# Performance work log

Hardware: AMD Instinct MI355X
Metric: run time of the kernel (lower is better)

## Reference

```python
import jax, jax.numpy as jnp
import numpy as np

H, HEADS, LAYERS = 512, 4, 3
HD = H // HEADS
FFN = 4 * H
B, S = 4, 2048
EPS = 1e-5
SCALE_BASE = 512.0
GAMMAS = (1.0 - np.exp(np.linspace(np.log(1.0 / 32.0), np.log(1.0 / 512.0), HEADS))).astype(np.float32)


def _xpos(x, downscale):
    # x: [B, heads, L, d]; standard XPOS rotary with per-dim decay scale
    L, d = x.shape[-2], x.shape[-1]
    half = d // 2
    s = (jnp.arange(half, dtype=jnp.float32) + 0.4 * d) / (1.4 * d)          # [half]
    pos = jnp.arange(L, dtype=jnp.float32)
    scale = s[None, :] ** (pos[:, None] / SCALE_BASE)                         # [L, half]
    inv_freq = 1.0 / (10000.0 ** (jnp.arange(half, dtype=jnp.float32) / half))
    ang = pos[:, None] * inv_freq[None, :]                                    # [L, half]
    if downscale:
        scale = 1.0 / scale
    sin_s = jnp.repeat(jnp.sin(ang) * scale, 2, axis=-1)                      # [L, d]
    cos_s = jnp.repeat(jnp.cos(ang) * scale, 2, axis=-1)
    x1, x2 = x[..., 0::2], x[..., 1::2]
    rot = jnp.stack([-x2, x1], axis=-1).reshape(x.shape)                      # rotate_every_two
    return x * cos_s + rot * sin_s


def _layernorm(x, w, b):
    m = x.mean(-1, keepdims=True)
    v = ((x - m) ** 2).mean(-1, keepdims=True)
    return (x - m) / jnp.sqrt(v + EPS) * w + b


def _decay_mask(L):
    n = jnp.arange(L)
    nm = n[:, None] - n[None, :]
    g = jnp.asarray(GAMMAS)                                                   # [heads]
    # D[h,n,m] = gamma_h^(n-m) for n>=m else 0
    return jnp.where((nm >= 0)[None], g[:, None, None] ** jnp.maximum(nm, 0)[None], 0.0)


def _msr(X, WQ, WK, WV, WG, WO, gnw, gnb, D):
    # X: [B,S,H]; WQ/WK/WV: [heads,H,HD]; D: [heads,S,S]
    Q = _xpos(jnp.einsum('bsh,nhd->bnsd', X, WQ), False)
    K = _xpos(jnp.einsum('bsh,nhd->bnsd', X, WK), True)
    V = jnp.einsum('bsh,nhd->bnsd', X, WV)
    A = jnp.einsum('bnsd,bntd->bnst', Q, K) * D[None]                          # decay-weighted retention
    Y = jnp.einsum('bnst,bntd->bnsd', A, V)                                    # [B,heads,S,HD]
    Y = jnp.transpose(Y, (0, 2, 1, 3))                                         # [B,S,heads,HD] (head-major concat)
    m = Y.mean(-1, keepdims=True)
    v = ((Y - m) ** 2).mean(-1, keepdims=True)
    Yn = ((Y - m) / jnp.sqrt(v + EPS)).reshape(X.shape[0], X.shape[1], H) * gnw + gnb  # GroupNorm(heads, H)
    G = X @ WG
    return (G * jax.nn.sigmoid(G) * Yn) @ WO                                   # swish gate + out proj


def setup_inputs() -> dict:
    key = jax.random.key(0)
    ks = jax.random.split(key, 10)
    rn = lambda k, shape, sc: jax.random.normal(k, shape, jnp.float32) * sc
    return {
        'X': rn(ks[0], (B, S, H), 1.0),
        'WQ': rn(ks[1], (LAYERS, HEADS, H, HD), 1.0 / H),
        'WK': rn(ks[2], (LAYERS, HEADS, H, HD), 1.0 / H),
        'WV': rn(ks[3], (LAYERS, HEADS, H, HD), 1.0 / H),
        'WG': rn(ks[4], (LAYERS, H, H), 1.0 / H),
        'WO': rn(ks[5], (LAYERS, H, H), 1.0 / H),
        'gn_w': jnp.ones((LAYERS, H), jnp.float32),
        'gn_b': jnp.zeros((LAYERS, H), jnp.float32),
        'ln1_w': jnp.ones((LAYERS, H), jnp.float32),
        'ln1_b': jnp.zeros((LAYERS, H), jnp.float32),
        'ln2_w': jnp.ones((LAYERS, H), jnp.float32),
        'ln2_b': jnp.zeros((LAYERS, H), jnp.float32),
        'ffn_w1': rn(ks[6], (LAYERS, H, FFN), (2.0 / (H + FFN)) ** 0.5),
        'ffn_b1': jnp.zeros((LAYERS, FFN), jnp.float32),
        'ffn_w2': rn(ks[7], (LAYERS, FFN, H), (2.0 / (H + FFN)) ** 0.5),
        'ffn_b2': jnp.zeros((LAYERS, H), jnp.float32),
    }


def reference(X, WQ, WK, WV, WG, WO, gn_w, gn_b, ln1_w, ln1_b, ln2_w, ln2_b, ffn_w1, ffn_b1, ffn_w2, ffn_b2):
    D = _decay_mask(X.shape[1])
    for l in range(LAYERS):
        Y = _msr(_layernorm(X, ln1_w[l], ln1_b[l]), WQ[l], WK[l], WV[l], WG[l], WO[l], gn_w[l], gn_b[l], D) + X
        Hn = _layernorm(Y, ln2_w[l], ln2_b[l])
        X = jax.nn.gelu(Hn @ ffn_w1[l] + ffn_b1[l], approximate=False) @ ffn_w2[l] + ffn_b2[l] + Y
    return X, jnp.einsum('bsh,bth->bst', X, X)
```

## Files before the change

### kernel.cpp

```cpp
#include <hip/hip_runtime.h>
#include <math.h>

#define HH 512
#define NHEADS 4
#define HD 128
#define HALF 64
#define FFND 2048
#define BB 4
#define SS 2048
#define NLAYERS 3
#define ROWS (BB*SS)
#define EPSF 1e-5f

typedef float f32x4 __attribute__((ext_vector_type(4)));
typedef __bf16 bf16x8 __attribute__((ext_vector_type(8)));

__device__ __forceinline__ unsigned short f2bf(float f) {
    union { float f; unsigned u; } v; v.f = f;
    unsigned r = (v.u + 0x7FFFu + ((v.u >> 16) & 1u)) >> 16;
    return (unsigned short)r;
}
__device__ __forceinline__ float bf2f(unsigned short h) {
    union { unsigned u; float f; } v; v.u = ((unsigned)h) << 16;
    return v.f;
}
__device__ __forceinline__ void gl16(const void* g, void* l) {
    __builtin_amdgcn_global_load_lds((const __attribute__((address_space(1))) void*)g,
                                     (__attribute__((address_space(3))) void*)l, 16, 0, 0);
}
__device__ __forceinline__ bf16x8 ld8(const void* p) { return *(const bf16x8*)p; }

__global__ void k_tables(float* __restrict__ cq, float* __restrict__ sq,
                         float* __restrict__ ck, float* __restrict__ sk) {
    int i = threadIdx.x;
    int s = blockIdx.x;
    float si   = ((float)i + 0.4f * (float)HD) / (1.4f * (float)HD);
    float scale = powf(si, (float)s / 512.0f);
    float invf = powf(10000.0f, -((float)i) / (float)HALF);
    float ang  = (float)s * invf;
    float c = cosf(ang), sn = sinf(ang);
    int idx = s * HALF + i;
    cq[idx] = c * scale;   sq[idx] = sn * scale;
    float is = 1.0f / scale;
    ck[idx] = c * is;      sk[idx] = sn * is;
}

__global__ __launch_bounds__(256) void k_wt(const float* __restrict__ src, unsigned short* __restrict__ dst,
                                            int K, int N) {
    __shared__ float T[32][33];
    int n0 = blockIdx.x * 32, k0 = blockIdx.y * 32;
    size_t mb = (size_t)blockIdx.z * (size_t)K * N;
    src += mb; dst += mb;
    int tx = threadIdx.x & 31, ty = threadIdx.x >> 5;
    #pragma unroll
    for (int i = 0; i < 4; ++i) {
        int r = ty + i * 8;
        T[r][tx] = src[(size_t)(k0 + r) * N + n0 + tx];
    }
    __syncthreads();
    #pragma unroll
    for (int i = 0; i < 4; ++i) {
        int r = ty + i * 8;
        dst[(size_t)(n0 + r) * K + k0 + tx] = f2bf(T[tx][r]);
    }
}

__global__ __launch_bounds__(256) void k_ln(const float* __restrict__ x, const float* __restrict__ w,
                                            const float* __restrict__ b, unsigned short* __restrict__ y) {
    int lane = threadIdx.x & 63;
    size_t row = (size_t)blockIdx.x * 4 + (threadIdx.x >> 6);
    const float4* xr = (const float4*)(x + row * HH);
    float4 v0 = xr[lane * 2];
    float4 v1 = xr[lane * 2 + 1];
    float s  = v0.x + v0.y + v0.z + v0.w + v1.x + v1.y + v1.z + v1.w;
    float ss = v0.x*v0.x + v0.y*v0.y + v0.z*v0.z + v0.w*v0.w
             + v1.x*v1.x + v1.y*v1.y + v1.z*v1.z + v1.w*v1.w;
    for (int off = 32; off > 0; off >>= 1) {
        s  += __shfl_xor(s, off);
        ss += __shfl_xor(ss, off);
    }
    float m   = s * (1.0f / HH);
    float var = ss * (1.0f / HH) - m * m;
    float inv = rsqrtf(var + EPSF);
    int h0 = lane * 8;
    float4 wa = *(const float4*)(w + h0);
    float4 wb = *(const float4*)(w + h0 + 4);
    float4 ba = *(const float4*)(b + h0);
    float4 bb2 = *(const float4*)(b + h0 + 4);
    unsigned short o0 = f2bf((v0.x - m) * inv * wa.x + ba.x);
    unsigned short o1 = f2bf((v0.y - m) * inv * wa.y + ba.y);
    unsigned short o2 = f2bf((v0.z - m) * inv * wa.z + ba.z);
    unsigned short o3 = f2bf((v0.w - m) * inv * wa.w + ba.w);
    unsigned short o4 = f2bf((v1.x - m) * inv * wb.x + bb2.x);
    unsigned short o5 = f2bf((v1.y - m) * inv * wb.y + bb2.y);
    unsigned short o6 = f2bf((v1.z - m) * inv * wb.z + bb2.z);
    unsigned short o7 = f2bf((v1.w - m) * inv * wb.w + bb2.w);
    uint4 pk;
    pk.x = o0 | ((unsigned)o1 << 16);
    pk.y = o2 | ((unsigned)o3 << 16);
    pk.z = o4 | ((unsigned)o5 << 16);
    pk.w = o6 | ((unsigned)o7 << 16);
    *(uint4*)(y + row * HH + h0) = pk;
}

__global__ __launch_bounds__(256) void k_xpos(unsigned short* __restrict__ Q, unsigned short* __restrict__ Kp,
    const float* __restrict__ cq, const float* __restrict__ sq,
    const float* __restrict__ ck, const float* __restrict__ sk) {
    int row = blockIdx.x, p = threadIdx.x;
    int s = row & (SS - 1), i = p & (HALF - 1);
    int ti = s * HALF + i;
    size_t off = (size_t)row * HH + p * 2;
    unsigned qv = *(unsigned*)(Q + off);
    float x1 = bf2f(qv & 0xffff), x2 = bf2f(qv >> 16);
    float c = cq[ti], sn = sq[ti];
    unsigned short e = f2bf(x1 * c - x2 * sn), o = f2bf(x2 * c + x1 * sn);
    *(unsigned*)(Q + off) = (unsigned)e | ((unsigned)o << 16);
    unsigned kv = *(unsigned*)(Kp + off);
    x1 = bf2f(kv & 0xffff); x2 = bf2f(kv >> 16);
    c = ck[ti]; sn = sk[ti];
    e = f2bf(x1 * c - x2 * sn); o = f2bf(x2 * c + x1 * sn);
    *(unsigned*)(Kp + off) = (unsigned)e | ((unsigned)o << 16);
}

__global__ __launch_bounds__(256) void k_ret(
    const unsigned short* __restrict__ Q, const unsigned short* __restrict__ K,
    const unsigned short* __restrict__ V, float* __restrict__ Y) {
    __shared__ __align__(16) char sm[57344];
    const int tid = threadIdx.x;
    const int lane = tid & 63, wid = tid >> 6;
    const int lcol = lane & 15, lrow = lane >> 4;
    const int xs = blockIdx.x, hn = blockIdx.y, b = blockIdx.z;
    const int s0 = xs * 64;
    const double la = -3.4657359027997265, lb = -6.238324625039508;
    const float gamma = (float)(1.0 - exp(la + (lb - la) * ((double)hn / 3.0)));
    const float l2g = log2f(gamma);
    const size_t rowbase = (size_t)b * SS;
    const size_t colbase = (size_t)hn * HD;
    #pragma unroll
    for (int c = 0; c < 4; ++c) {
        int chunk = wid * 4 + c;
        int r = chunk * 4 + lrow;
        int w = ((lane & 15) * 16) ^ ((r & 7) << 4);
        gl16((const char*)Q + ((rowbase + s0 + r) * HH + colbase) * 2 + w, sm + chunk * 1024);
    }
    float gr[4], gni[4];
    #pragma unroll
    for (int j = 0; j < 4; ++j) { gr[j] = exp2f(l2g * (float)j); gni[j] = exp2f(-l2g * (16.0f * j)); }
    f32x4 accy[8];
    #pragma unroll
    for (int i = 0; i < 8; ++i) accy[i] = f32x4{0.f, 0.f, 0.f, 0.f};
    const int nt = xs + 1;
    for (int t = 0; t < nt; ++t) {
        const int t0 = t * 64;
        __syncthreads();
        #pragma unroll
        for (int c = 0; c < 4; ++c) {
            int chunk = wid * 4 + c;
            int r = chunk * 4 + lrow;
            int w = ((lane & 15) * 16) ^ ((r & 7) << 4);
            gl16((const char*)K + ((rowbase + t0 + r) * HH + colbase) * 2 + w, sm + 16384 + chunk * 1024);
        }
        {
            const int tt = tid & 63, q4 = tid >> 6;
            #pragma unroll
            for (int j = 0; j < 4; ++j) {
                const int d0 = q4 * 32 + j * 8;
                uint4 vv = *(const uint4*)((const char*)V + ((rowbase + t0 + tt) * HH + colbase + d0) * 2);
                const unsigned short* vs = (const unsigned short*)&vv;
                #pragma unroll
                for (int e = 0; e < 8; ++e) {
                    int d = d0 + e;
                    *(unsigned short*)(sm + 32768 + d * 128 + ((tt * 2) ^ ((d & 7) << 4))) = vs[e];
                }
            }
        }
        __syncthreads();
        f32x4 pacc[4];
        #pragma unroll
        for (int i = 0; i < 4; ++i) pacc[i] = f32x4{0.f, 0.f, 0.f, 0.f};
        #pragma unroll
        for (int kk = 0; kk < 4; ++kk) {
            int ar = wid * 16 + lcol;
            bf16x8 af = ld8(sm + ar * 256 + ((kk * 64 + lrow * 16) ^ ((ar & 7) << 4)));
            #pragma unroll
            for (int nn = 0; nn < 4; ++nn) {
                int br = nn * 16 + lcol;
                bf16x8 bf = ld8(sm + 16384 + br * 256 + ((kk * 64 + lrow * 16) ^ ((br & 7) << 4)));
                pacc[nn] = __builtin_amdgcn_mfma_f32_16x16x32_bf16(af, bf, pacc[nn], 0, 0, 0);
            }
        }
        const int e0 = (s0 - t0) + wid * 16 + lrow * 4 - lcol;
        const float G0 = exp2f(l2g * (float)e0);
        #pragma unroll
        for (int nn = 0; nn < 4; ++nn) {
            #pragma unroll
            for (int j = 0; j < 4; ++j) {
                const int delta = e0 + j - nn * 16;
                const float dd = (delta >= 0) ? (G0 * gr[j] * gni[nn]) : 0.0f;
                const float pv = pacc[nn][j] * dd;
                const int pr = wid * 16 + lrow * 4 + j;
                const int pc = nn * 16 + lcol;
                *(unsigned short*)(sm + 49152 + pr * 128 + ((pc * 2) ^ ((pr & 7) << 4))) = f2bf(pv);
            }
        }
        #pragma unroll
        for (int ks = 0; ks < 2; ++ks) {
            int ar = wid * 16 + lcol;
            bf16x8 pf = ld8(sm + 49152 + ar * 128 + ((ks * 64 + lrow * 16) ^ ((ar & 7) << 4)));
            #pragma unroll
            for (int nn = 0; nn < 8; ++nn) {
                int dr = nn * 16 + lcol;
                bf16x8 vf = ld8(sm + 32768 + dr * 128 + ((ks * 64 + lrow * 16) ^ ((dr & 7) << 4)));
                accy[nn] = __builtin_amdgcn_mfma_f32_16x16x32_bf16(pf, vf, accy[nn], 0, 0, 0);
            }
        }
    }
    #pragma unroll
    for (int nn = 0; nn < 8; ++nn)
        #pragma unroll
        for (int j = 0; j < 4; ++j) {
            size_t row = rowbase + s0 + wid * 16 + lrow * 4 + j;
            Y[row * HH + colbase + nn * 16 + lcol] = accy[nn][j];
        }
}

__global__ __launch_bounds__(256) void k_gate(
    const float* __restrict__ Yr, const unsigned short* __restrict__ G,
    const float* __restrict__ gw, const float* __restrict__ gb,
    unsigned short* __restrict__ E) {
    int lane = threadIdx.x & 63;
    int grp  = blockIdx.x * 4 + (threadIdx.x >> 6);
    int row = grp >> 2, nh = grp & 3;
    size_t off = (size_t)row * HH + nh * HD + lane * 2;
    float2 v = *(const float2*)(Yr + off);
    float s = v.x + v.y, ss = v.x * v.x + v.y * v.y;
    for (int o = 32; o > 0; o >>= 1) {
        s  += __shfl_xor(s, o);
        ss += __shfl_xor(ss, o);
    }
    float m   = s * (1.0f / HD);
    float var = ss * (1.0f / HD) - m * m;
    float inv = rsqrtf(var + EPSF);
    int h = nh * HD + lane * 2;
    unsigned gv = *(const unsigned*)(G + off);
    float g0 = bf2f(gv & 0xffff), g1 = bf2f(gv >> 16);
    float2 w2 = *(const float2*)(gw + h), b2 = *(const float2*)(gb + h);
    float yn0 = (v.x - m) * inv * w2.x + b2.x;
    float yn1 = (v.y - m) * inv * w2.y + b2.y;
    float e0v = g0 / (1.0f + expf(-g0)) * yn0;
    float e1v = g1 / (1.0f + expf(-g1)) * yn1;
    *(unsigned*)(E + off) = (unsigned)f2bf(e0v) | ((unsigned)f2bf(e1v) << 16);
}

__global__ __launch_bounds__(256) void k_cast(const float* __restrict__ x, unsigned short* __restrict__ y) {
    size_t i = ((size_t)blockIdx.x * 256 + threadIdx.x) * 8;
    float4 a = *(const float4*)(x + i), c = *(const float4*)(x + i + 4);
    uint4 pk;
    pk.x = f2bf(a.x) | ((unsigned)f2bf(a.y) << 16);
    pk.y = f2bf(a.z) | ((unsigned)f2bf(a.w) << 16);
    pk.z = f2bf(c.x) | ((unsigned)f2bf(c.y) << 16);
    pk.w = f2bf(c.z) | ((unsigned)f2bf(c.w) << 16);
    *(uint4*)(y + i) = pk;
}

template<int EPI, int OUTBF>
__global__ __launch_bounds__(256) void k_mm(
    const unsigned short* __restrict__ A, const unsigned short* __restrict__ Bt,
    void* __restrict__ Cv, const float* __restrict__ bias, const float* __restrict__ Rs,
    int M, int N, int K, size_t aB, size_t bB, size_t cB) {
    __shared__ __align__(16) char sm[16384];
    const int tid = threadIdx.x;
    const int lane = tid & 63, wid = tid >> 6;
    const int wr = wid >> 1, wc = wid & 1;
    const int lcol = lane & 15, lrow = lane >> 4;
    const size_t m0 = (size_t)blockIdx.x * 128, n0 = (size_t)blockIdx.y * 128;
    const char* Ab = (const char*)(A + (size_t)blockIdx.z * aB);
    const char* Bb = (const char*)(Bt + (size_t)blockIdx.z * bB);
    f32x4 acc[4][4];
    #pragma unroll
    for (int i = 0; i < 4; ++i)
        #pragma unroll
        for (int j = 0; j < 4; ++j) acc[i][j] = f32x4{0.f, 0.f, 0.f, 0.f};
    for (int k0 = 0; k0 < K; k0 += 32) {
        __syncthreads();
        #pragma unroll
        for (int c = 0; c < 2; ++c) {
            int chunk = wid * 2 + c;
            int r = chunk * 16 + (lane >> 2);
            int w = ((lane & 3) ^ (r & 3)) << 4;
            gl16(Ab + ((size_t)(m0 + r) * K + k0) * 2 + w, sm + chunk * 1024);
            gl16(Bb + ((size_t)(n0 + r) * K + k0) * 2 + w, sm + 8192 + chunk * 1024);
        }
        __syncthreads();
        bf16x8 af[4], bfr[4];
        #pragma unroll
        for (int m = 0; m < 4; ++m) {
            int r = wr * 64 + m * 16 + lcol;
            af[m] = ld8(sm + r * 64 + ((lrow * 16) ^ ((r & 3) << 4)));
        }
        #pragma unroll
        for (int n2 = 0; n2 < 4; ++n2) {
            int r = wc * 64 + n2 * 16 + lcol;
            bfr[n2] = ld8(sm + 8192 + r * 64 + ((lrow * 16) ^ ((r & 3) << 4)));
        }
        #pragma unroll
        for (int m = 0; m < 4; ++m)
            #pragma unroll
            for (int n2 = 0; n2 < 4; ++n2)
                acc[m][n2] = __builtin_amdgcn_mfma_f32_16x16x32_bf16(af[m], bfr[n2], acc[m][n2], 0, 0, 0);
    }
    float* Cf = (float*)Cv + (size_t)blockIdx.z * cB;
    unsigned short* Cb = (unsigned short*)Cv + (size_t)blockIdx.z * cB;
    const float* Rb = (EPI >= 2) ? (Rs + (size_t)blockIdx.z * cB) : nullptr;
    #pragma unroll
    for (int m = 0; m < 4; ++m) {
        #pragma unroll
        for (int n2 = 0; n2 < 4; ++n2) {
            size_t col = n0 + wc * 64 + n2 * 16 + lcol;
            float bc = (EPI == 1 || EPI == 2) ? bias[col] : 0.0f;
            #pragma unroll
            for (int j = 0; j < 4; ++j) {
                size_t row = m0 + wr * 64 + m * 16 + lrow * 4 + j;
                float v = acc[m][n2][j];
                if (EPI == 1) { v += bc; v = 0.5f * v * (1.0f + erff(v * 0.70710678118654752f)); }
                else if (EPI == 2) v += bc + Rb[row * N + col];
                else if (EPI == 3) v += Rb[row * N + col];
                if (OUTBF) Cb[row * N + col] = f2bf(v);
                else       Cf[row * N + col] = v;
            }
        }
    }
}

extern "C" void kernel_launch(void* const* d_in, const int* in_sizes, int n_in,
                              void* d_out, int out_size, void* d_ws, size_t ws_size,
                              hipStream_t stream) {
    const float* X0  = (const float*)d_in[0];
    const float* WQ  = (const float*)d_in[1];
    const float* WK  = (const float*)d_in[2];
    const float* WV  = (const float*)d_in[3];
    const float* WG  = (const float*)d_in[4];
    const float* WO  = (const float*)d_in[5];
    const float* gnw = (const float*)d_in[6];
    const float* gnb = (const float*)d_in[7];
    const float* l1w = (const float*)d_in[8];
    const float* l1b = (const float*)d_in[9];
    const float* l2w = (const float*)d_in[10];
    const float* l2b = (const float*)d_in[11];
    const float* fw1 = (const float*)d_in[12];
    const float* fb1 = (const float*)d_in[13];
    const float* fw2 = (const float*)d_in[14];
    const float* fb2 = (const float*)d_in[15];
    float* outX = (float*)d_out;
    float* outG = outX + (size_t)ROWS * HH;

    char* wp = (char*)d_ws;
    auto take = [&](size_t bytes) { char* p = wp; wp += (bytes + 255) & ~(size_t)255; return p; };
    float* cq = (float*)take((size_t)SS * HALF * 4);
    float* sq = (float*)take((size_t)SS * HALF * 4);
    float* ck = (float*)take((size_t)SS * HALF * 4);
    float* sk = (float*)take((size_t)SS * HALF * 4);
    unsigned short* WQt = (unsigned short*)take((size_t)NLAYERS * HH * HH * 2);
    unsigned short* WKt = (unsigned short*)take((size_t)NLAYERS * HH * HH * 2);
    unsigned short* WVt = (unsigned short*)take((size_t)NLAYERS * HH * HH * 2);
    unsigned short* WGt = (unsigned short*)take((size_t)NLAYERS * HH * HH * 2);
    unsigned short* WOt = (unsigned short*)take((size_t)NLAYERS * HH * HH * 2);
    unsigned short* F1t = (unsigned short*)take((size_t)NLAYERS * HH * FFND * 2);
    unsigned short* F2t = (unsigned short*)take((size_t)NLAYERS * HH * FFND * 2);
    unsigned short* Xn  = (unsigned short*)take((size_t)ROWS * HH * 2);
    unsigned short* Qb  = (unsigned short*)take((size_t)ROWS * HH * 2);
    unsigned short* Kb  = (unsigned short*)take((size_t)ROWS * HH * 2);
    unsigned short* Vb  = (unsigned short*)take((size_t)ROWS * HH * 2);
    float* Yr   = (float*)take((size_t)ROWS * HH * 4);
    float* Y2   = (float*)take((size_t)ROWS * HH * 4);
    float* Xbuf = (float*)take((size_t)ROWS * HH * 4);
    unsigned short* Hb = (unsigned short*)take((size_t)ROWS * FFND * 2);
    unsigned short* Gb = Kb;
    unsigned short* Eb = Qb;
    unsigned short* Xb = Xn;

    k_tables<<<SS, HALF, 0, stream>>>(cq, sq, ck, sk);
    k_wt<<<dim3(4, 16, 12), 256, 0, stream>>>(WQ, WQt, HH, HD);
    k_wt<<<dim3(4, 16, 12), 256, 0, stream>>>(WK, WKt, HH, HD);
    k_wt<<<dim3(4, 16, 12), 256, 0, stream>>>(WV, WVt, HH, HD);
    k_wt<<<dim3(16, 16, 3), 256, 0, stream>>>(WG, WGt, HH, HH);
    k_wt<<<dim3(16, 16, 3), 256, 0, stream>>>(WO, WOt, HH, HH);
    k_wt<<<dim3(64, 16, 3), 256, 0, stream>>>(fw1, F1t, HH, FFND);
    k_wt<<<dim3(16, 64, 3), 256, 0, stream>>>(fw2, F2t, FFND, HH);

    const float* curX = X0;
    for (int l = 0; l < NLAYERS; ++l) {
        const unsigned short* Bq = WQt + (size_t)l * HH * HH;
        const unsigned short* Bk = WKt + (size_t)l * HH * HH;
        const unsigned short* Bv = WVt + (size_t)l * HH * HH;
        const unsigned short* Bg = WGt + (size_t)l * HH * HH;
        const unsigned short* Bo = WOt + (size_t)l * HH * HH;
        const unsigned short* B1 = F1t + (size_t)l * HH * FFND;
        const unsigned short* B2 = F2t + (size_t)l * HH * FFND;
        k_ln<<<ROWS / 4, 256, 0, stream>>>(curX, l1w + l * HH, l1b + l * HH, Xn);
        dim3 g1(ROWS / 128, HH / 128, 1);
        k_mm<0, 1><<<g1, 256, 0, stream>>>(Xn, Bq, Qb, nullptr, nullptr, ROWS, HH, HH, 0, 0, 0);
        k_mm<0, 1><<<g1, 256, 0, stream>>>(Xn, Bk, Kb, nullptr, nullptr, ROWS, HH, HH, 0, 0, 0);
        k_mm<0, 1><<<g1, 256, 0, stream>>>(Xn, Bv, Vb, nullptr, nullptr, ROWS, HH, HH, 0, 0, 0);
        k_xpos<<<ROWS, 256, 0, stream>>>(Qb, Kb, cq, sq, ck, sk);
        k_ret<<<dim3(SS / 64, NHEADS, BB), 256, 0, stream>>>(Qb, Kb, Vb, Yr);
        k_mm<0, 1><<<g1, 256, 0, stream>>>(Xn, Bg, Gb, nullptr, nullptr, ROWS, HH, HH, 0, 0, 0);
        k_gate<<<ROWS, 256, 0, stream>>>(Yr, Gb, gnw + l * HH, gnb + l * HH, Eb);
        k_mm<3, 0><<<g1, 256, 0, stream>>>(Eb, Bo, Y2, nullptr, curX, ROWS, HH, HH, 0, 0, 0);
        k_ln<<<ROWS / 4, 256, 0, stream>>>(Y2, l2w + l * HH, l2b + l * HH, Xn);
        dim3 g2(ROWS / 128, FFND / 128, 1);
        k_mm<1, 1><<<g2, 256, 0, stream>>>(Xn, B1, Hb, fb1 + (size_t)l * FFND, nullptr, ROWS, FFND, HH, 0, 0, 0);
        float* newX = (l == NLAYERS - 1) ? outX : Xbuf;
        k_mm<2, 0><<<g1, 256, 0, stream>>>(Hb, B2, newX, fb2 + (size_t)l * HH, Y2, ROWS, HH, FFND, 0, 0, 0);
        curX = newX;
    }
    k_cast<<<ROWS * HH / (256 * 8), 256, 0, stream>>>(outX, Xb);
    dim3 g3(SS / 128, SS / 128, BB);
    k_mm<0, 0><<<g3, 256, 0, stream>>>(Xb, Xb, outG, nullptr, nullptr, SS, SS, HH,
                                       (size_t)SS * HH, (size_t)SS * HH, (size_t)SS * SS);
}
```

Before: 1.038 ms.

## Fuse QKVG projections into one GEMM and rework retention kernel with 32x32 MFMA

Concatenates the Q, K, V and gate weights into one [2048x512] matrix, so a single wide GEMM replaces four launches and writes an interleaved QKVG buffer. The retention kernel now uses 128-thread blocks with Q held in registers and 32x32x16 MFMAs. V is loaded straight into LDS and read back with ds_read_b64_tr_b16 transposed reads instead of a scalar scatter transpose. Causal blocks are launched in reverse order so the heaviest tiles start first. The aim is to cut launch overhead and the LDS transpose cost, at the price of a wider-stride layout and higher register pressure.

```diff
diff --git a/kernel.cpp b/kernel.cpp
--- a/kernel.cpp
+++ b/kernel.cpp
@@ -11,9 +11,12 @@
 #define NLAYERS 3
 #define ROWS (BB*SS)
 #define EPSF 1e-5f
+#define QKVGW 2048
 
 typedef float f32x4 __attribute__((ext_vector_type(4)));
+typedef float f32x16 __attribute__((ext_vector_type(16)));
 typedef __bf16 bf16x8 __attribute__((ext_vector_type(8)));
+typedef unsigned u32x2 __attribute__((ext_vector_type(2)));
 
 __device__ __forceinline__ unsigned short f2bf(float f) {
     union { float f; unsigned u; } v; v.f = f;
@@ -29,6 +32,14 @@
                                      (__attribute__((address_space(3))) void*)l, 16, 0, 0);
 }
 __device__ __forceinline__ bf16x8 ld8(const void* p) { return *(const bf16x8*)p; }
+__device__ __forceinline__ unsigned laddr(void* p) {
+    return (unsigned)(size_t)(__attribute__((address_space(3))) char*)p;
+}
+__device__ __forceinline__ u32x2 tr8(unsigned a) {
+    u32x2 r;
+    asm volatile("ds_read_b64_tr_b16 %0, %1" : "=v"(r) : "v"(a));
+    return r;
+}
 
 __global__ void k_tables(float* __restrict__ cq, float* __restrict__ sq,
                          float* __restrict__ ck, float* __restrict__ sk) {
@@ -46,11 +57,12 @@
 }
 
 __global__ __launch_bounds__(256) void k_wt(const float* __restrict__ src, unsigned short* __restrict__ dst,
-                                            int K, int N) {
+                                            int K, int N, int zn, size_t sL, size_t sZ) {
     __shared__ float T[32][33];
     int n0 = blockIdx.x * 32, k0 = blockIdx.y * 32;
-    size_t mb = (size_t)blockIdx.z * (size_t)K * N;
-    src += mb; dst += mb;
+    int z = blockIdx.z;
+    src += (size_t)z * (size_t)K * N;
+    dst += (size_t)(z / zn) * sL + (size_t)(z % zn) * sZ;
     int tx = threadIdx.x & 31, ty = threadIdx.x >> 5;
     #pragma unroll
     for (int i = 0; i < 4; ++i) {
@@ -87,145 +99,160 @@
     float4 wb = *(const float4*)(w + h0 + 4);
     float4 ba = *(const float4*)(b + h0);
     float4 bb2 = *(const float4*)(b + h0 + 4);
-    unsigned short o0 = f2bf((v0.x - m) * inv * wa.x + ba.x);
-    unsigned short o1 = f2bf((v0.y - m) * inv * wa.y + ba.y);
-    unsigned short o2 = f2bf((v0.z - m) * inv * wa.z + ba.z);
-    unsigned short o3 = f2bf((v0.w - m) * inv * wa.w + ba.w);
-    unsigned short o4 = f2bf((v1.x - m) * inv * wb.x + bb2.x);
-    unsigned short o5 = f2bf((v1.y - m) * inv * wb.y + bb2.y);
-    unsigned short o6 = f2bf((v1.z - m) * inv * wb.z + bb2.z);
-    unsigned short o7 = f2bf((v1.w - m) * inv * wb.w + bb2.w);
     uint4 pk;
-    pk.x = o0 | ((unsigned)o1 << 16);
-    pk.y = o2 | ((unsigned)o3 << 16);
-    pk.z = o4 | ((unsigned)o5 << 16);
-    pk.w = o6 | ((unsigned)o7 << 16);
+    pk.x = f2bf((v0.x - m) * inv * wa.x + ba.x) | ((unsigned)f2bf((v0.y - m) * inv * wa.y + ba.y) << 16);
+    pk.y = f2bf((v0.z - m) * inv * wa.z + ba.z) | ((unsigned)f2bf((v0.w - m) * inv * wa.w + ba.w) << 16);
+    pk.z = f2bf((v1.x - m) * inv * wb.x + bb2.x) | ((unsigned)f2bf((v1.y - m) * inv * wb.y + bb2.y) << 16);
+    pk.w = f2bf((v1.z - m) * inv * wb.z + bb2.z) | ((unsigned)f2bf((v1.w - m) * inv * wb.w + bb2.w) << 16);
     *(uint4*)(y + row * HH + h0) = pk;
 }
 
-__global__ __launch_bounds__(256) void k_xpos(unsigned short* __restrict__ Q, unsigned short* __restrict__ Kp,
+__global__ __launch_bounds__(256) void k_xpos(unsigned short* __restrict__ QG,
     const float* __restrict__ cq, const float* __restrict__ sq,
     const float* __restrict__ ck, const float* __restrict__ sk) {
     int row = blockIdx.x, p = threadIdx.x;
-    int s = row & (SS - 1), i = p & (HALF - 1);
+    int s = row & (SS - 1), n = p >> 6, i = p & 63;
     int ti = s * HALF + i;
-    size_t off = (size_t)row * HH + p * 2;
-    unsigned qv = *(unsigned*)(Q + off);
+    size_t qo = (size_t)row * QKVGW + n * HD + i * 2;
+    unsigned qv = *(unsigned*)(QG + qo);
     float x1 = bf2f(qv & 0xffff), x2 = bf2f(qv >> 16);
     float c = cq[ti], sn = sq[ti];
-    unsigned short e = f2bf(x1 * c - x2 * sn), o = f2bf(x2 * c + x1 * sn);
-    *(unsigned*)(Q + off) = (unsigned)e | ((unsigned)o << 16);
-    unsigned kv = *(unsigned*)(Kp + off);
+    *(unsigned*)(QG + qo) = (unsigned)f2bf(x1 * c - x2 * sn) | ((unsigned)f2bf(x2 * c + x1 * sn) << 16);
+    size_t ko = qo + 512;
+    unsigned kv = *(unsigned*)(QG + ko);
     x1 = bf2f(kv & 0xffff); x2 = bf2f(kv >> 16);
     c = ck[ti]; sn = sk[ti];
-    e = f2bf(x1 * c - x2 * sn); o = f2bf(x2 * c + x1 * sn);
-    *(unsigned*)(Kp + off) = (unsigned)e | ((unsigned)o << 16);
-}
-
-__global__ __launch_bounds__(256) void k_ret(
-    const unsigned short* __restrict__ Q, const unsigned short* __restrict__ K,
-    const unsigned short* __restrict__ V, float* __restrict__ Y) {
-    __shared__ __align__(16) char sm[57344];
+    *(unsigned*)(QG + ko) = (unsigned)f2bf(x1 * c - x2 * sn) | ((unsigned)f2bf(x2 * c + x1 * sn) << 16);
+}
+
+__global__ __launch_bounds__(128, 2) void k_ret(
+    const unsigned short* __restrict__ QG, float* __restrict__ Y) {
+    __shared__ __align__(16) char sm[40960];
     const int tid = threadIdx.x;
-    const int lane = tid & 63, wid = tid >> 6;
-    const int lcol = lane & 15, lrow = lane >> 4;
-    const int xs = blockIdx.x, hn = blockIdx.y, b = blockIdx.z;
+    const int lane = tid & 63, wv = tid >> 6;
+    const int l31 = lane & 31, g2 = lane >> 5;
+    const int b4 = (lane >> 4) & 1;
+    const int xs = (int)gridDim.x - 1 - (int)blockIdx.x;
+    const int hn = blockIdx.y, b = blockIdx.z;
     const int s0 = xs * 64;
     const double la = -3.4657359027997265, lb = -6.238324625039508;
     const float gamma = (float)(1.0 - exp(la + (lb - la) * ((double)hn / 3.0)));
     const float l2g = log2f(gamma);
     const size_t rowbase = (size_t)b * SS;
-    const size_t colbase = (size_t)hn * HD;
-    #pragma unroll
-    for (int c = 0; c < 4; ++c) {
-        int chunk = wid * 4 + c;
-        int r = chunk * 4 + lrow;
-        int w = ((lane & 15) * 16) ^ ((r & 7) << 4);
-        gl16((const char*)Q + ((rowbase + s0 + r) * HH + colbase) * 2 + w, sm + chunk * 1024);
-    }
-    float gr[4], gni[4];
-    #pragma unroll
-    for (int j = 0; j < 4; ++j) { gr[j] = exp2f(l2g * (float)j); gni[j] = exp2f(-l2g * (16.0f * j)); }
-    f32x4 accy[8];
-    #pragma unroll
-    for (int i = 0; i < 8; ++i) accy[i] = f32x4{0.f, 0.f, 0.f, 0.f};
+    const int qcol = hn * HD, kcol = 512 + hn * HD, vcol = 1024 + hn * HD;
+    const char* Gp = (const char*)QG;
+
+    const int srow = s0 + wv * 32 + l31;
+    bf16x8 qf[8];
+    #pragma unroll
+    for (int kc = 0; kc < 8; ++kc)
+        qf[kc] = ld8(QG + (rowbase + srow) * QKVGW + qcol + kc * 16 + g2 * 8);
+
+    float gq[4], gj[4];
+    #pragma unroll
+    for (int q = 0; q < 4; ++q) { gq[q] = exp2f(-l2g * (8.0f * q)); gj[q] = exp2f(-l2g * (float)q); }
+    const float gt32m = exp2f(-l2g * 32.0f);
+
+    f32x16 accy[4];
+    #pragma unroll
+    for (int d = 0; d < 4; ++d)
+        #pragma unroll
+        for (int e = 0; e < 16; ++e) accy[d][e] = 0.0f;
+
+    const int sloc = wv * 32 + l31;
+    const int ssw = (sloc & 7) << 4;
+    const int r15 = (l31 & 15) << 4;
+    const unsigned vbase = laddr(sm + 16384) + b4 * 2048 + g2 * 256 + (lane & 15) * 2;
     const int nt = xs + 1;
+
     for (int t = 0; t < nt; ++t) {
         const int t0 = t * 64;
         __syncthreads();
         #pragma unroll
-        for (int c = 0; c < 4; ++c) {
-            int chunk = wid * 4 + c;
-            int r = chunk * 4 + lrow;
-            int w = ((lane & 15) * 16) ^ ((r & 7) << 4);
-            gl16((const char*)K + ((rowbase + t0 + r) * HH + colbase) * 2 + w, sm + 16384 + chunk * 1024);
-        }
-        {
-            const int tt = tid & 63, q4 = tid >> 6;
+        for (int c = 0; c < 8; ++c) {
+            int chunk = wv * 8 + c;
+            int r = chunk * 4 + (lane >> 4);
+            int w = ((lane & 15) * 16) ^ ((r & 15) << 4);
+            gl16(Gp + ((rowbase + t0 + r) * QKVGW + kcol) * 2 + w, sm + chunk * 1024);
+        }
+        #pragma unroll
+        for (int c = 0; c < 8; ++c) {
+            int chunk = wv * 8 + c;
+            int slot = chunk * 64 + lane;
+            int sub = slot >> 3, w8 = slot & 7;
+            int db = sub >> 4, tb = sub & 15;
+            int tl = tb * 4 + (w8 >> 1);
+            int d  = db * 16 + (w8 & 1) * 8;
+            gl16(Gp + ((rowbase + t0 + tl) * QKVGW + vcol + d) * 2, sm + 16384 + chunk * 1024);
+        }
+        __syncthreads();
+        f32x16 pacc0, pacc1;
+        #pragma unroll
+        for (int e = 0; e < 16; ++e) { pacc0[e] = 0.0f; pacc1[e] = 0.0f; }
+        #pragma unroll
+        for (int kc = 0; kc < 8; ++kc) {
+            bf16x8 k0 = ld8(sm + l31 * 256 + ((kc * 32 + g2 * 16) ^ r15));
+            bf16x8 k1 = ld8(sm + (32 + l31) * 256 + ((kc * 32 + g2 * 16) ^ r15));
+            pacc0 = __builtin_amdgcn_mfma_f32_32x32x16_bf16(k0, qf[kc], pacc0, 0, 0, 0);
+            pacc1 = __builtin_amdgcn_mfma_f32_32x32x16_bf16(k1, qf[kc], pacc1, 0, 0, 0);
+        }
+        const float G0 = exp2f(l2g * (float)(srow - t0 - g2 * 4));
+        #pragma unroll
+        for (int tb2 = 0; tb2 < 2; ++tb2) {
+            const float gb = tb2 ? gt32m : 1.0f;
             #pragma unroll
-            for (int j = 0; j < 4; ++j) {
-                const int d0 = q4 * 32 + j * 8;
-                uint4 vv = *(const uint4*)((const char*)V + ((rowbase + t0 + tt) * HH + colbase + d0) * 2);
-                const unsigned short* vs = (const unsigned short*)&vv;
-                #pragma unroll
-                for (int e = 0; e < 8; ++e) {
-                    int d = d0 + e;
-                    *(unsigned short*)(sm + 32768 + d * 128 + ((tt * 2) ^ ((d & 7) << 4))) = vs[e];
-                }
+            for (int q = 0; q < 4; ++q) {
+                unsigned short u0, u1, u2, u3;
+                int tbase = t0 + tb2 * 32 + q * 8 + g2 * 4;
+                float base = G0 * gb * gq[q];
+                float p0 = (tb2 ? pacc1 : pacc0)[q * 4 + 0];
+                float p1 = (tb2 ? pacc1 : pacc0)[q * 4 + 1];
+                float p2 = (tb2 ? pacc1 : pacc0)[q * 4 + 2];
+                float p3 = (tb2 ? pacc1 : pacc0)[q * 4 + 3];
+                u0 = f2bf((srow >= tbase + 0) ? p0 * base * gj[0] : 0.0f);
+                u1 = f2bf((srow >= tbase + 1) ? p1 * base * gj[1] : 0.0f);
+                u2 = f2bf((srow >= tbase + 2) ? p2 * base * gj[2] : 0.0f);
+                u3 = f2bf((srow >= tbase + 3) ? p3 * base * gj[3] : 0.0f);
+                u32x2 pk2;
+                pk2.x = (unsigned)u0 | ((unsigned)u1 << 16);
+                pk2.y = (unsigned)u2 | ((unsigned)u3 << 16);
+                *(u32x2*)(sm + 32768 + ((sloc * 128 + tb2 * 64 + q * 16 + g2 * 8) ^ ssw)) = pk2;
             }
         }
-        __syncthreads();
-        f32x4 pacc[4];
-        #pragma unroll
-        for (int i = 0; i < 4; ++i) pacc[i] = f32x4{0.f, 0.f, 0.f, 0.f};
-        #pragma unroll
-        for (int kk = 0; kk < 4; ++kk) {
-            int ar = wid * 16 + lcol;
-            bf16x8 af = ld8(sm + ar * 256 + ((kk * 64 + lrow * 16) ^ ((ar & 7) << 4)));
+        bf16x8 pf[4];
+        #pragma unroll
+        for (int tc = 0; tc < 4; ++tc)
+            pf[tc] = ld8(sm + 32768 + ((sloc * 128 + tc * 32 + g2 * 16) ^ ssw));
+        #pragma unroll
+        for (int dblk = 0; dblk < 4; ++dblk) {
+            u32x2 va[4], vb[4];
             #pragma unroll
-            for (int nn = 0; nn < 4; ++nn) {
-                int br = nn * 16 + lcol;
-                bf16x8 bf = ld8(sm + 16384 + br * 256 + ((kk * 64 + lrow * 16) ^ ((br & 7) << 4)));
-                pacc[nn] = __builtin_amdgcn_mfma_f32_16x16x32_bf16(af, bf, pacc[nn], 0, 0, 0);
+            for (int tc = 0; tc < 4; ++tc) {
+                unsigned a0 = vbase + dblk * 4096 + tc * 512;
+                va[tc] = tr8(a0);
+                vb[tc] = tr8(a0 + 128);
             }
-        }
-        const int e0 = (s0 - t0) + wid * 16 + lrow * 4 - lcol;
-        const float G0 = exp2f(l2g * (float)e0);
-        #pragma unroll
-        for (int nn = 0; nn < 4; ++nn) {
+            asm volatile("s_waitcnt lgkmcnt(0)" ::: "memory");
+            __builtin_amdgcn_sched_barrier(0);
             #pragma unroll
-            for (int j = 0; j < 4; ++j) {
-                const int delta = e0 + j - nn * 16;
-                const float dd = (delta >= 0) ? (G0 * gr[j] * gni[nn]) : 0.0f;
-                const float pv = pacc[nn][j] * dd;
-                const int pr = wid * 16 + lrow * 4 + j;
-                const int pc = nn * 16 + lcol;
-                *(unsigned short*)(sm + 49152 + pr * 128 + ((pc * 2) ^ ((pr & 7) << 4))) = f2bf(pv);
+            for (int tc = 0; tc < 4; ++tc) {
+                union { u32x2 u[2]; bf16x8 v; } cvt;
+                cvt.u[0] = va[tc]; cvt.u[1] = vb[tc];
+                accy[dblk] = __builtin_amdgcn_mfma_f32_32x32x16_bf16(pf[tc], cvt.v, accy[dblk], 0, 0, 0);
             }
         }
-        #pragma unroll
-        for (int ks = 0; ks < 2; ++ks) {
-            int ar = wid * 16 + lcol;
-            bf16x8 pf = ld8(sm + 49152 + ar * 128 + ((ks * 64 + lrow * 16) ^ ((ar & 7) << 4)));
-            #pragma unroll
-            for (int nn = 0; nn < 8; ++nn) {
-                int dr = nn * 16 + lcol;
-                bf16x8 vf = ld8(sm + 32768 + dr * 128 + ((ks * 64 + lrow * 16) ^ ((dr & 7) << 4)));
-                accy[nn] = __builtin_amdgcn_mfma_f32_16x16x32_bf16(pf, vf, accy[nn], 0, 0, 0);
-            }
-        }
-    }
-    #pragma unroll
-    for (int nn = 0; nn < 8; ++nn)
-        #pragma unroll
-        for (int j = 0; j < 4; ++j) {
-            size_t row = rowbase + s0 + wid * 16 + lrow * 4 + j;
-            Y[row * HH + colbase + nn * 16 + lcol] = accy[nn][j];
+    }
+    #pragma unroll
+    for (int dblk = 0; dblk < 4; ++dblk)
+        #pragma unroll
+        for (int rg = 0; rg < 16; ++rg) {
+            int sl2 = s0 + wv * 32 + (rg & 3) + (rg >> 2) * 8 + g2 * 4;
+            Y[(rowbase + sl2) * HH + hn * HD + dblk * 32 + l31] = accy[dblk][rg];
         }
 }
 
 __global__ __launch_bounds__(256) void k_gate(
-    const float* __restrict__ Yr, const unsigned short* __restrict__ G,
+    const float* __restrict__ Yr, const unsigned short* __restrict__ QG,
     const float* __restrict__ gw, const float* __restrict__ gb,
     unsigned short* __restrict__ E) {
     int lane = threadIdx.x & 63;
@@ -242,7 +269,7 @@
     float var = ss * (1.0f / HD) - m * m;
     float inv = rsqrtf(var + EPSF);
     int h = nh * HD + lane * 2;
-    unsigned gv = *(const unsigned*)(G + off);
+    unsigned gv = *(const unsigned*)(QG + (size_t)row * QKVGW + 1536 + nh * HD + lane * 2);
     float g0 = bf2f(gv & 0xffff), g1 = bf2f(gv >> 16);
     float2 w2 = *(const float2*)(gw + h), b2 = *(const float2*)(gb + h);
     float yn0 = (v.x - m) * inv * w2.x + b2.x;
@@ -360,52 +387,41 @@
     float* sq = (float*)take((size_t)SS * HALF * 4);
     float* ck = (float*)take((size_t)SS * HALF * 4);
     float* sk = (float*)take((size_t)SS * HALF * 4);
-    unsigned short* WQt = (unsigned short*)take((size_t)NLAYERS * HH * HH * 2);
-    unsigned short* WKt = (unsigned short*)take((size_t)NLAYERS * HH * HH * 2);
-    unsigned short* WVt = (unsigned short*)take((size_t)NLAYERS * HH * HH * 2);
-    unsigned short* WGt = (unsigned short*)take((size_t)NLAYERS * HH * HH * 2);
+    unsigned short* Wcat = (unsigned short*)take((size_t)NLAYERS * QKVGW * HH * 2);
     unsigned short* WOt = (unsigned short*)take((size_t)NLAYERS * HH * HH * 2);
     unsigned short* F1t = (unsigned short*)take((size_t)NLAYERS * HH * FFND * 2);
     unsigned short* F2t = (unsigned short*)take((size_t)NLAYERS * HH * FFND * 2);
     unsigned short* Xn  = (unsigned short*)take((size_t)ROWS * HH * 2);
-    unsigned short* Qb  = (unsigned short*)take((size_t)ROWS * HH * 2);
-    unsigned short* Kb  = (unsigned short*)take((size_t)ROWS * HH * 2);
-    unsigned short* Vb  = (unsigned short*)take((size_t)ROWS * HH * 2);
+    unsigned short* QKVG = (unsigned short*)take((size_t)ROWS * QKVGW * 2);
+    unsigned short* Eb  = (unsigned short*)take((size_t)ROWS * HH * 2);
     float* Yr   = (float*)take((size_t)ROWS * HH * 4);
     float* Y2   = (float*)take((size_t)ROWS * HH * 4);
     float* Xbuf = (float*)take((size_t)ROWS * HH * 4);
     unsigned short* Hb = (unsigned short*)take((size_t)ROWS * FFND * 2);
-    unsigned short* Gb = Kb;
-    unsigned short* Eb = Qb;
     unsigned short* Xb = Xn;
 
     k_tables<<<SS, HALF, 0, stream>>>(cq, sq, ck, sk);
-    k_wt<<<dim3(4, 16, 12), 256, 0, stream>>>(WQ, WQt, HH, HD);
-    k_wt<<<dim3(4, 16, 12), 256, 0, stream>>>(WK, WKt, HH, HD);
-    k_wt<<<dim3(4, 16, 12), 256, 0, stream>>>(WV, WVt, HH, HD);
-    k_wt<<<dim3(16, 16, 3), 256, 0, stream>>>(WG, WGt, HH, HH);
-    k_wt<<<dim3(16, 16, 3), 256, 0, stream>>>(WO, WOt, HH, HH);
-    k_wt<<<dim3(64, 16, 3), 256, 0, stream>>>(fw1, F1t, HH, FFND);
-    k_wt<<<dim3(16, 64, 3), 256, 0, stream>>>(fw2, F2t, FFND, HH);
+    k_wt<<<dim3(4, 16, 12), 256, 0, stream>>>(WQ, Wcat, HH, HD, 4, (size_t)QKVGW * HH, (size_t)HD * HH);
+    k_wt<<<dim3(4, 16, 12), 256, 0, stream>>>(WK, Wcat + (size_t)512 * HH, HH, HD, 4, (size_t)QKVGW * HH, (size_t)HD * HH);
+    k_wt<<<dim3(4, 16, 12), 256, 0, stream>>>(WV, Wcat + (size_t)1024 * HH, HH, HD, 4, (size_t)QKVGW * HH, (size_t)HD * HH);
+    k_wt<<<dim3(16, 16, 3), 256, 0, stream>>>(WG, Wcat + (size_t)1536 * HH, HH, HH, 1, (size_t)QKVGW * HH, 0);
+    k_wt<<<dim3(16, 16, 3), 256, 0, stream>>>(WO, WOt, HH, HH, 1, (size_t)HH * HH, 0);
+    k_wt<<<dim3(64, 16, 3), 256, 0, stream>>>(fw1, F1t, HH, FFND, 1, (size_t)HH * FFND, 0);
+    k_wt<<<dim3(16, 64, 3), 256, 0, stream>>>(fw2, F2t, FFND, HH, 1, (size_t)FFND * HH, 0);
 
     const float* curX = X0;
     for (int l = 0; l < NLAYERS; ++l) {
-        const unsigned short* Bq = WQt + (size_t)l * HH * HH;
-        const unsigned short* Bk = WKt + (size_t)l * HH * HH;
-        const unsigned short* Bv = WVt + (size_t)l * HH * HH;
-        const unsigned short* Bg = WGt + (size_t)l * HH * HH;
+        const unsigned short* Bc = Wcat + (size_t)l * QKVGW * HH;
         const unsigned short* Bo = WOt + (size_t)l * HH * HH;
         const unsigned short* B1 = F1t + (size_t)l * HH * FFND;
         const unsigned short* B2 = F2t + (size_t)l * HH * FFND;
         k_ln<<<ROWS / 4, 256, 0, stream>>>(curX, l1w + l * HH, l1b + l * HH, Xn);
+        dim3 gq(ROWS / 128, QKVGW / 128, 1);
+        k_mm<0, 1><<<gq, 256, 0, stream>>>(Xn, Bc, QKVG, nullptr, nullptr, ROWS, QKVGW, HH, 0, 0, 0);
+        k_xpos<<<ROWS, 256, 0, stream>>>(QKVG, cq, sq, ck, sk);
+        k_ret<<<dim3(SS / 64, NHEADS, BB), 128, 0, stream>>>(QKVG, Yr);
+        k_gate<<<ROWS, 256, 0, stream>>>(Yr, QKVG, gnw + l * HH, gnb + l * HH, Eb);
         dim3 g1(ROWS / 128, HH / 128, 1);
-        k_mm<0, 1><<<g1, 256, 0, stream>>>(Xn, Bq, Qb, nullptr, nullptr, ROWS, HH, HH, 0, 0, 0);
-        k_mm<0, 1><<<g1, 256, 0, stream>>>(Xn, Bk, Kb, nullptr, nullptr, ROWS, HH, HH, 0, 0, 0);
-        k_mm<0, 1><<<g1, 256, 0, stream>>>(Xn, Bv, Vb, nullptr, nullptr, ROWS, HH, HH, 0, 0, 0);
-        k_xpos<<<ROWS, 256, 0, stream>>>(Qb, Kb, cq, sq, ck, sk);
-        k_ret<<<dim3(SS / 64, NHEADS, BB), 256, 0, stream>>>(Qb, Kb, Vb, Yr);
-        k_mm<0, 1><<<g1, 256, 0, stream>>>(Xn, Bg, Gb, nullptr, nullptr, ROWS, HH, HH, 0, 0, 0);
-        k_gate<<<ROWS, 256, 0, stream>>>(Yr, Gb, gnw + l * HH, gnb + l * HH, Eb);
         k_mm<3, 0><<<g1, 256, 0, stream>>>(Eb, Bo, Y2, nullptr, curX, ROWS, HH, HH, 0, 0, 0);
         k_ln<<<ROWS / 4, 256, 0, stream>>>(Y2, l2w + l * HH, l2b + l * HH, Xn);
         dim3 g2(ROWS / 128, FFND / 128, 1);
```

New measurement: 930.2 us. 10.4% less time.
